# Kernel optimization log

Hardware: AMD Instinct MI355X
Metric: run time of the kernel (lower is better)

Reference implementation:

```python
import jax, jax.numpy as jnp
import numpy as np

G = 4  # number of groups


def _group_vals(h, shift, Ua, Ua1, Ua2, Ua3):
    # h: [B, H]; Ua: [g, H/g, r]; Ua1/2/3: [g, r, H/g]
    B, H = h.shape
    hg = h.reshape(B, G, H // G)
    if shift:
        # torch index = rotate-left by `shift`: new group j reads old group (j+shift)%g
        hg = jnp.roll(hg, -shift, axis=1)
    t = jnp.einsum('bgd,gdr->bgr', hg, Ua)  # shared low-rank projection
    proj = lambda M: jnp.einsum('bgr,grd->bgd', t, M).reshape(B, H)
    return proj(Ua1), proj(Ua2), proj(Ua3)


def setup_inputs() -> dict:
    key = jax.random.key(0)
    ks = jax.random.split(key, 24)
    B, I, H, wR = 8192, 1024, 1024, 256
    hg = H // G
    r01, r23 = 64, 32
    d = {}
    d['x'] = jax.random.normal(ks[0], (B, I), dtype=jnp.float32)
    d['h'] = jax.random.normal(ks[1], (B, H), dtype=jnp.float32)
    d['W'] = 0.1 * jax.random.normal(ks[2], (I, wR), dtype=jnp.float32)
    d['W1'] = 0.1 * jax.random.normal(ks[3], (wR, H), dtype=jnp.float32)
    d['W2'] = 0.1 * jax.random.normal(ks[4], (wR, H), dtype=jnp.float32)
    d['W3'] = 0.1 * jax.random.normal(ks[5], (wR, H), dtype=jnp.float32)
    d['U'] = 0.1 * jax.random.normal(ks[6], (G, hg, r01), dtype=jnp.float32)
    d['U1'] = 0.1 * jax.random.normal(ks[7], (G, r01, hg), dtype=jnp.float32)
    d['U2'] = 0.1 * jax.random.normal(ks[8], (G, r01, hg), dtype=jnp.float32)
    d['U3'] = 0.1 * jax.random.normal(ks[9], (G, r01, hg), dtype=jnp.float32)
    d['UU'] = 0.1 * jax.random.normal(ks[10], (G, hg, r01), dtype=jnp.float32)
    d['UU1'] = 0.1 * jax.random.normal(ks[11], (G, r01, hg), dtype=jnp.float32)
    d['UU2'] = 0.1 * jax.random.normal(ks[12], (G, r01, hg), dtype=jnp.float32)
    d['UU3'] = 0.1 * jax.random.normal(ks[13], (G, r01, hg), dtype=jnp.float32)
    d['UUU'] = 0.1 * jax.random.normal(ks[14], (G, hg, r23), dtype=jnp.float32)
    d['UUU1'] = 0.1 * jax.random.normal(ks[15], (G, r23, hg), dtype=jnp.float32)
    d['UUU2'] = 0.1 * jax.random.normal(ks[16], (G, r23, hg), dtype=jnp.float32)
    d['UUU3'] = 0.1 * jax.random.normal(ks[17], (G, r23, hg), dtype=jnp.float32)
    d['UUUU'] = 0.1 * jax.random.normal(ks[18], (G, hg, r23), dtype=jnp.float32)
    d['UUUU1'] = 0.1 * jax.random.normal(ks[19], (G, r23, hg), dtype=jnp.float32)
    d['UUUU2'] = 0.1 * jax.random.normal(ks[20], (G, r23, hg), dtype=jnp.float32)
    d['UUUU3'] = 0.1 * jax.random.normal(ks[21], (G, r23, hg), dtype=jnp.float32)
    d['bias_r'] = jnp.ones((1, H), dtype=jnp.float32)
    d['bias_gate'] = jnp.ones((1, H), dtype=jnp.float32)
    d['bias_update'] = jnp.ones((1, H), dtype=jnp.float32)
    return d


def reference(x, h, W, W1, W2, W3, U, U1, U2, U3, UU, UU1, UU2, UU3,
              UUU, UUU1, UUU2, UUU3, UUUU, UUUU1, UUUU2, UUUU3,
              bias_r, bias_gate, bias_update):
    u1, u2, u3 = _group_vals(h, 0, U, U1, U2, U3)
    uu1, uu2, uu3 = _group_vals(h, 1, UU, UU1, UU2, UU3)
    uuu1, uuu2, uuu3 = _group_vals(h, 2, UUU, UUU1, UUU2, UUU3)
    uuuu1, uuuu2, uuuu3 = _group_vals(h, 3, UUUU, UUUU1, UUUU2, UUUU3)
    xw = x @ W  # [B, wRank]
    w1, w2, w3 = xw @ W1, xw @ W2, xw @ W3
    r = jax.nn.sigmoid(w1 + u1 + uu1 + uuu1 + uuuu1 + bias_r)
    z = jax.nn.sigmoid(w2 + u2 + uu2 + uuu2 + uuuu2 + bias_gate)
    c_tilda = jnp.tanh(w3 + r * (u3 + uu3 + uuu3 + uuuu3) + bias_update)
    return z * h + (1.0 - z) * c_tilda
```

## Files before the change

kernel.cpp:

```cpp
#include <hip/hip_runtime.h>

typedef short bf16x8 __attribute__((ext_vector_type(8)));
typedef float f32x4 __attribute__((ext_vector_type(4)));

__device__ __forceinline__ unsigned short f2bf(float f) {
  union { float f; unsigned u; } c; c.f = f;
  unsigned u = c.u;
  u += 0x7FFFu + ((u >> 16) & 1u);
  return (unsigned short)(u >> 16);
}
__device__ __forceinline__ float bf2f(unsigned short h) {
  union { unsigned u; float f; } c; c.u = ((unsigned)h) << 16;
  return c.f;
}
__device__ __forceinline__ void split2(float v, unsigned short& hi, unsigned short& lo) {
  union { float f; unsigned u; } c; c.f = v;
  unsigned uh = c.u & 0xFFFF0000u;
  hi = (unsigned short)(uh >> 16);
  union { unsigned u; float f; } d; d.u = uh;
  lo = f2bf(v - d.f);
}
__device__ __forceinline__ void gload16(const void* g, void* l) {
  __builtin_amdgcn_global_load_lds((const __attribute__((address_space(1))) void*)g,
                                   (__attribute__((address_space(3))) void*)l, 16, 0, 0);
}
__device__ __forceinline__ float sigm(float x) { return 1.0f / (1.0f + __expf(-x)); }
__device__ __forceinline__ float tanha(float x) { return 1.0f - 2.0f / (1.0f + __expf(2.0f * x)); }

__global__ __launch_bounds__(256) void s123(
    const float* __restrict__ W,
    const float* __restrict__ U, const float* __restrict__ UU,
    const float* __restrict__ UUU, const float* __restrict__ UUUU,
    const float* __restrict__ W1, const float* __restrict__ W2, const float* __restrict__ W3,
    const float* __restrict__ A1, const float* __restrict__ A2, const float* __restrict__ A3,
    const float* __restrict__ B1, const float* __restrict__ B2, const float* __restrict__ B3,
    const float* __restrict__ C1, const float* __restrict__ C2, const float* __restrict__ C3,
    const float* __restrict__ D1, const float* __restrict__ D2, const float* __restrict__ D3,
    unsigned short* __restrict__ Wt, unsigned short* __restrict__ Bg,
    unsigned short* __restrict__ Bt) {
  int gidx = blockIdx.x * 256 + threadIdx.x;
  if (gidx < 262144) {
    int idx = gidx;
    int n = idx >> 10, k = idx & 1023;
    Wt[idx] = f2bf(W[k * 256 + n]);
  } else if (gidx < 458752) {
    int idx = gidx - 262144;
    int g = idx / 49152;
    int rem = idx - g * 49152;
    int n = rem >> 8, k = rem & 255;
    int jj = 0, rr = n;
#pragma unroll
    for (int s = 0; s < 3; ++s) {
      int w = (((g - jj) & 3) < 2) ? 64 : 32;
      if (rr >= w) { rr -= w; ++jj; }
    }
    int v = (g - jj) & 3;
    int rv = (v < 2) ? 64 : 32;
    const float* M = (v == 0) ? U : (v == 1) ? UU : (v == 2) ? UUU : UUUU;
    Bg[idx] = f2bf(M[(jj * 256 + k) * rv + rr]);
  } else {
    int idx = gidx - 458752;
    int j = idx / (1024 * 704);
    int rem = idx - j * (1024 * 704);
    int n = rem / 704, k = rem - n * 704;
    int p = n >> 8, c = n & 255;
    float val = 0.0f;
    if (k < 512) {
      int kk = k & 255;
      if (p == 0)      val = W1[kk * 1024 + j * 256 + c];
      else if (p == 1) val = W2[kk * 1024 + j * 256 + c];
      else if (p == 2) val = W3[kk * 1024 + j * 256 + c];
    } else if (p != 2) {
      int k2 = k - 512;
      int v, off, rv;
      if (k2 < 64)       { v = 0; off = 0;   rv = 64; }
      else if (k2 < 128) { v = 1; off = 64;  rv = 64; }
      else if (k2 < 160) { v = 2; off = 128; rv = 32; }
      else               { v = 3; off = 160; rv = 32; }
      int r = k2 - off;
      int pp = (p == 3) ? 2 : p;
      const float* M;
      if (v == 0)      M = (pp == 0) ? A1 : (pp == 1) ? A2 : A3;
      else if (v == 1) M = (pp == 0) ? B1 : (pp == 1) ? B2 : B3;
      else if (v == 2) M = (pp == 0) ? C1 : (pp == 1) ? C2 : C3;
      else             M = (pp == 0) ? D1 : (pp == 1) ? D2 : D3;
      val = M[(j * rv + r) * 256 + c];
    }
    Bt[idx] = f2bf(val);
  }
}

__global__ __launch_bounds__(256) void g1_xw(const float* __restrict__ x,
                                             const unsigned short* __restrict__ Wt,
                                             unsigned short* __restrict__ Abuf) {
  __shared__ char lds[49152];
  const int tid = threadIdx.x, lane = tid & 63, wid = tid >> 6;
  const int mb = blockIdx.x, nb = blockIdx.y;
  const int wn = wid;
  f32x4 acc[2][2] = {};
  float4 xr[2];
  const int r0 = tid >> 4, f4c = tid & 15;
  const float* xbase = x + (size_t)(mb * 32) * 1024 + f4c * 4;

  auto loadX = [&](int kt) {
#pragma unroll
    for (int q = 0; q < 2; ++q)
      xr[q] = *(const float4*)(xbase + (size_t)(q * 16 + r0) * 1024 + kt * 64);
  };
  auto writeA = [&](int buf) {
#pragma unroll
    for (int q = 0; q < 2; ++q) {
      int row = q * 16 + r0;
      float4 v = xr[q];
      unsigned short h0, h1, h2, h3, l0, l1, l2, l3;
      split2(v.x, h0, l0); split2(v.y, h1, l1);
      split2(v.z, h2, l2); split2(v.w, h3, l3);
      int ba = row * 128 + ((f4c * 8) ^ ((row & 7) << 4));
      *(uint2*)(lds + buf * 4096 + ba) =
          make_uint2(((unsigned)h1 << 16) | h0, ((unsigned)h3 << 16) | h2);
      *(uint2*)(lds + 8192 + buf * 4096 + ba) =
          make_uint2(((unsigned)l1 << 16) | l0, ((unsigned)l3 << 16) | l2);
    }
  };
  auto stageB = [&](int kt, int buf) {
#pragma unroll
    for (int it = 0; it < 4; ++it) {
      int nloc = it * 32 + wid * 8 + (lane >> 3);
      const char* src = (const char*)Wt + (size_t)(nb * 128 + nloc) * 2048 + kt * 128
                        + (((lane & 7) * 16) ^ ((nloc & 7) << 4));
      gload16(src, lds + 16384 + buf * 16384 + it * 4096 + wid * 1024);
    }
  };

  loadX(0); stageB(0, 0); writeA(0);
  __syncthreads();
#pragma unroll 2
  for (int kt = 0; kt < 16; ++kt) {
    int buf = kt & 1;
    if (kt < 15) { loadX(kt + 1); stageB(kt + 1, buf ^ 1); }
    const char* hA = lds + buf * 4096;
    const char* lA = lds + 8192 + buf * 4096;
    const char* bB = lds + 16384 + buf * 16384;
#pragma unroll
    for (int ks = 0; ks < 2; ++ks) {
      bf16x8 ah[2], al[2], b[2];
#pragma unroll
      for (int mf = 0; mf < 2; ++mf) {
        int mloc = mf * 16 + (lane & 15);
        int ka = (ks * 64 + (lane >> 4) * 16) ^ ((mloc & 7) << 4);
        ah[mf] = *(const bf16x8*)(hA + mloc * 128 + ka);
        al[mf] = *(const bf16x8*)(lA + mloc * 128 + ka);
      }
#pragma unroll
      for (int nf = 0; nf < 2; ++nf) {
        int nloc = wn * 32 + nf * 16 + (lane & 15);
        int kb = (ks * 64 + (lane >> 4) * 16) ^ ((nloc & 7) << 4);
        b[nf] = *(const bf16x8*)(bB + nloc * 128 + kb);
      }
#pragma unroll
      for (int mf = 0; mf < 2; ++mf)
#pragma unroll
        for (int nf = 0; nf < 2; ++nf) {
          acc[mf][nf] = __builtin_amdgcn_mfma_f32_16x16x32_bf16(ah[mf], b[nf], acc[mf][nf], 0, 0, 0);
          acc[mf][nf] = __builtin_amdgcn_mfma_f32_16x16x32_bf16(al[mf], b[nf], acc[mf][nf], 0, 0, 0);
        }
    }
    if (kt < 15) writeA(buf ^ 1);
    __syncthreads();
  }
#pragma unroll
  for (int mf = 0; mf < 2; ++mf)
#pragma unroll
    for (int nf = 0; nf < 2; ++nf)
#pragma unroll
      for (int r = 0; r < 4; ++r) {
        int row = mb * 32 + mf * 16 + (lane >> 4) * 4 + r;
        int col = nb * 128 + wn * 32 + nf * 16 + (lane & 15);
        float val = acc[mf][nf][r];
        unsigned short hi, lo;
        split2(val, hi, lo);
        Abuf[(size_t)row * 1280 + col] = hi;
        Abuf[(size_t)row * 1280 + 256 + col] = lo;
      }
}

__global__ __launch_bounds__(256) void g2_t(const float* __restrict__ h,
                                            const unsigned short* __restrict__ Bg,
                                            unsigned short* __restrict__ Abuf) {
  __shared__ char lds[65536];
  const int tid = threadIdx.x, lane = tid & 63, wid = tid >> 6;
  const int mb = blockIdx.x, g = blockIdx.y;
  const int wm = wid >> 1, wn = wid & 1;
  f32x4 acc[2][6] = {};
  float4 hr[4];
  const int r0 = tid >> 4, f4c = tid & 15;
  const float* hbase = h + (size_t)(mb * 64) * 1024 + g * 256 + f4c * 4;

  auto loadH = [&](int kt) {
#pragma unroll
    for (int q = 0; q < 4; ++q)
      hr[q] = *(const float4*)(hbase + (size_t)(q * 16 + r0) * 1024 + kt * 64);
  };
  auto writeA = [&](int buf) {
#pragma unroll
    for (int q = 0; q < 4; ++q) {
      int row = q * 16 + r0;
      float4 v = hr[q];
      int ba = row * 128 + ((f4c * 8) ^ ((row & 7) << 4));
      *(uint2*)(lds + buf * 8192 + ba) =
          make_uint2(((unsigned)f2bf(v.y) << 16) | f2bf(v.x),
                     ((unsigned)f2bf(v.w) << 16) | f2bf(v.z));
    }
  };
  auto stageB = [&](int kt, int buf) {
#pragma unroll
    for (int it = 0; it < 6; ++it) {
      int nloc = it * 32 + wid * 8 + (lane >> 3);
      const char* src = (const char*)Bg + (size_t)(g * 192 + nloc) * 512 + kt * 128
                        + (((lane & 7) * 16) ^ ((nloc & 7) << 4));
      gload16(src, lds + 16384 + buf * 24576 + it * 4096 + wid * 1024);
    }
  };

  loadH(0); stageB(0, 0); writeA(0);
  __syncthreads();
#pragma unroll
  for (int kt = 0; kt < 4; ++kt) {
    int buf = kt & 1;
    if (kt < 3) { loadH(kt + 1); stageB(kt + 1, buf ^ 1); }
    const char* cA = lds + buf * 8192;
    const char* cB = lds + 16384 + buf * 24576;
#pragma unroll
    for (int ks = 0; ks < 2; ++ks) {
      bf16x8 a[2], b[6];
#pragma unroll
      for (int mf = 0; mf < 2; ++mf) {
        int mloc = wm * 32 + mf * 16 + (lane & 15);
        int ka = (ks * 64 + (lane >> 4) * 16) ^ ((mloc & 7) << 4);
        a[mf] = *(const bf16x8*)(cA + mloc * 128 + ka);
      }
#pragma unroll
      for (int nf = 0; nf < 6; ++nf) {
        int nloc = wn * 96 + nf * 16 + (lane & 15);
        int kb = (ks * 64 + (lane >> 4) * 16) ^ ((nloc & 7) << 4);
        b[nf] = *(const bf16x8*)(cB + nloc * 128 + kb);
      }
#pragma unroll
      for (int mf = 0; mf < 2; ++mf)
#pragma unroll
        for (int nf = 0; nf < 6; ++nf)
          acc[mf][nf] = __builtin_amdgcn_mfma_f32_16x16x32_bf16(a[mf], b[nf], acc[mf][nf], 0, 0, 0);
    }
    if (kt < 3) writeA(buf ^ 1);
    __syncthreads();
  }
#pragma unroll
  for (int mf = 0; mf < 2; ++mf)
#pragma unroll
    for (int nf = 0; nf < 6; ++nf) {
      int n = wn * 96 + nf * 16 + (lane & 15);
      int jj = 0, rr = n;
#pragma unroll
      for (int s = 0; s < 3; ++s) {
        int w = (((g - jj) & 3) < 2) ? 64 : 32;
        if (rr >= w) { rr -= w; ++jj; }
      }
      int v = (g - jj) & 3;
      int offv = (v < 2) ? (v << 6) : (64 + (v << 5));
      int col = 512 + jj * 192 + offv + rr;
#pragma unroll
      for (int r = 0; r < 4; ++r) {
        int row = mb * 64 + wm * 32 + mf * 16 + (lane >> 4) * 4 + r;
        Abuf[(size_t)row * 1280 + col] = f2bf(acc[mf][nf][r]);
      }
    }
}

__global__ __launch_bounds__(256) void g3_main(const unsigned short* __restrict__ Abuf,
                                               const unsigned short* __restrict__ Bt,
                                               const float* __restrict__ h,
                                               const float* __restrict__ bias_r,
                                               const float* __restrict__ bias_g,
                                               const float* __restrict__ bias_u,
                                               float* __restrict__ out) {
  __shared__ char lds[65536];
  const int tid = threadIdx.x, lane = tid & 63, wid = tid >> 6;
  const int mb = blockIdx.x, nb = blockIdx.y, j = blockIdx.z;
  const int wm = wid >> 1, wn = wid & 1;
  f32x4 acc[4][4] = {};

  const char* AbufB = (const char*)Abuf + (size_t)mb * 128 * 2560;
  const char* BtB = (const char*)Bt + (size_t)j * 1441792;
  int thrA[4], thrB[4], dstOff[4];
#pragma unroll
  for (int it = 0; it < 4; ++it) {
    int mloc = wid * 32 + it * 8 + (lane >> 3);
    int swz = ((lane & 7) * 16) ^ ((mloc & 7) << 4);
    thrA[it] = mloc * 2560 + swz;
    int cb2 = (mloc >> 6) & 1, p = (mloc >> 4) & 3, c16 = mloc & 15;
    thrB[it] = (p * 256 + nb * 32 + cb2 * 16 + c16) * 1408 + swz;
    dstOff[it] = wid * 4096 + it * 1024;
  }
  const char* pA[4][2];
  const char* pB[4][2];
#pragma unroll
  for (int mf = 0; mf < 4; ++mf) {
    int mloc = wm * 64 + mf * 16 + (lane & 15);
#pragma unroll
    for (int ks = 0; ks < 2; ++ks) {
      int ka = (ks * 64 + (lane >> 4) * 16) ^ ((mloc & 7) << 4);
      pA[mf][ks] = lds + mloc * 128 + ka;
    }
  }
#pragma unroll
  for (int p = 0; p < 4; ++p) {
    int nloc = wn * 64 + p * 16 + (lane & 15);
#pragma unroll
    for (int ks = 0; ks < 2; ++ks) {
      int kb = (ks * 64 + (lane >> 4) * 16) ^ ((nloc & 7) << 4);
      pB[p][ks] = lds + 32768 + nloc * 128 + kb;
    }
  }

  auto stage = [&](int kt, int buf) {
    int colb2 = (kt < 8) ? kt * 128 : (1024 + j * 384 + (kt - 8) * 128);
#pragma unroll
    for (int it = 0; it < 4; ++it)
      gload16(AbufB + colb2 + thrA[it], lds + buf * 16384 + dstOff[it]);
#pragma unroll
    for (int it = 0; it < 4; ++it)
      gload16(BtB + kt * 128 + thrB[it], lds + 32768 + buf * 16384 + dstOff[it]);
  };

  stage(0, 0);
  __syncthreads();
#pragma unroll
  for (int kt = 0; kt < 11; ++kt) {
    int buf = kt & 1;
    if (kt < 10) stage(kt + 1, buf ^ 1);
    __builtin_amdgcn_s_setprio(1);
#pragma unroll
    for (int ks = 0; ks < 2; ++ks) {
      bf16x8 a[4];
#pragma unroll
      for (int mf = 0; mf < 4; ++mf)
        a[mf] = *(const bf16x8*)(pA[mf][ks] + buf * 16384);
#pragma unroll
      for (int p = 0; p < 4; ++p) {
        if (p == 2 && kt >= 8) continue;
        if (p == 3 && kt < 8) continue;
        bf16x8 b = *(const bf16x8*)(pB[p][ks] + buf * 16384);
#pragma unroll
        for (int mf = 0; mf < 4; ++mf)
          acc[mf][p] = __builtin_amdgcn_mfma_f32_16x16x32_bf16(a[mf], b, acc[mf][p], 0, 0, 0);
      }
    }
    __builtin_amdgcn_s_setprio(0);
    __syncthreads();
  }
  int cg = j * 256 + nb * 32 + wn * 16 + (lane & 15);
  float br = bias_r[cg], bg = bias_g[cg], bu = bias_u[cg];
#pragma unroll
  for (int mf = 0; mf < 4; ++mf)
#pragma unroll
    for (int r = 0; r < 4; ++r) {
      int row = mb * 128 + wm * 64 + mf * 16 + (lane >> 4) * 4 + r;
      float p0 = acc[mf][0][r], p1 = acc[mf][1][r];
      float p2 = acc[mf][2][r], p3 = acc[mf][3][r];
      float rr = sigm(p0 + br);
      float zz = sigm(p1 + bg);
      float ct = tanha(p2 + rr * p3 + bu);
      float hv = h[(size_t)row * 1024 + cg];
      out[(size_t)row * 1024 + cg] = zz * hv + (1.0f - zz) * ct;
    }
}

extern "C" void kernel_launch(void* const* d_in, const int* in_sizes, int n_in,
                              void* d_out, int out_size, void* d_ws, size_t ws_size,
                              hipStream_t stream) {
  const float* x   = (const float*)d_in[0];
  const float* h   = (const float*)d_in[1];
  const float* W   = (const float*)d_in[2];
  const float* W1  = (const float*)d_in[3];
  const float* W2  = (const float*)d_in[4];
  const float* W3  = (const float*)d_in[5];
  const float* U   = (const float*)d_in[6];
  const float* U1  = (const float*)d_in[7];
  const float* U2  = (const float*)d_in[8];
  const float* U3  = (const float*)d_in[9];
  const float* UU   = (const float*)d_in[10];
  const float* UU1  = (const float*)d_in[11];
  const float* UU2  = (const float*)d_in[12];
  const float* UU3  = (const float*)d_in[13];
  const float* UUU   = (const float*)d_in[14];
  const float* UUU1  = (const float*)d_in[15];
  const float* UUU2  = (const float*)d_in[16];
  const float* UUU3  = (const float*)d_in[17];
  const float* UUUU   = (const float*)d_in[18];
  const float* UUUU1  = (const float*)d_in[19];
  const float* UUUU2  = (const float*)d_in[20];
  const float* UUUU3  = (const float*)d_in[21];
  const float* bias_r = (const float*)d_in[22];
  const float* bias_g = (const float*)d_in[23];
  const float* bias_u = (const float*)d_in[24];

  char* ws = (char*)d_ws;
  unsigned short* Abuf = (unsigned short*)(ws);
  unsigned short* Wt   = (unsigned short*)(ws + 20971520);
  unsigned short* Bg   = (unsigned short*)(ws + 21495808);
  unsigned short* Bt   = (unsigned short*)(ws + 21889024);
  float* out = (float*)d_out;

  s123<<<13056, 256, 0, stream>>>(W, U, UU, UUU, UUUU,
                                  W1, W2, W3, U1, U2, U3, UU1, UU2, UU3,
                                  UUU1, UUU2, UUU3, UUUU1, UUUU2, UUUU3,
                                  Wt, Bg, Bt);
  g1_xw<<<dim3(256, 2), 256, 0, stream>>>(x, Wt, Abuf);
  g2_t<<<dim3(128, 4), 256, 0, stream>>>(h, Bg, Abuf);
  g3_main<<<dim3(64, 8, 4), 256, 0, stream>>>(Abuf, Bt, h, bias_r, bias_g, bias_u, out);
}
```

Baseline: 99.98 us.

## Pack weight tiles contiguously, drop zero-padded B slots, and pipeline with explicit waitcnts

```diff
diff --git a/kernel.cpp b/kernel.cpp
--- a/kernel.cpp
+++ b/kernel.cpp
@@ -37,7 +37,7 @@
     const float* __restrict__ C1, const float* __restrict__ C2, const float* __restrict__ C3,
     const float* __restrict__ D1, const float* __restrict__ D2, const float* __restrict__ D3,
     unsigned short* __restrict__ Wt, unsigned short* __restrict__ Bg,
-    unsigned short* __restrict__ Bt) {
+    unsigned short* __restrict__ Btp) {
   int gidx = blockIdx.x * 256 + threadIdx.x;
   if (gidx < 262144) {
     int idx = gidx;
@@ -60,33 +60,37 @@
     Bg[idx] = f2bf(M[(jj * 256 + k) * rv + rr]);
   } else {
     int idx = gidx - 458752;
-    int j = idx / (1024 * 704);
-    int rem = idx - j * (1024 * 704);
-    int n = rem / 704, k = rem - n * 704;
-    int p = n >> 8, c = n & 255;
-    float val = 0.0f;
-    if (k < 512) {
-      int kk = k & 255;
-      if (p == 0)      val = W1[kk * 1024 + j * 256 + c];
-      else if (p == 1) val = W2[kk * 1024 + j * 256 + c];
-      else if (p == 2) val = W3[kk * 1024 + j * 256 + c];
-    } else if (p != 2) {
-      int k2 = k - 512;
-      int v, off, rv;
-      if (k2 < 64)       { v = 0; off = 0;   rv = 64; }
-      else if (k2 < 128) { v = 1; off = 64;  rv = 64; }
-      else if (k2 < 160) { v = 2; off = 128; rv = 32; }
-      else               { v = 3; off = 160; rv = 32; }
-      int r = k2 - off;
-      int pp = (p == 3) ? 2 : p;
+    int j  = idx / 540672;
+    int r1 = idx - j * 540672;
+    int kt = r1 / 49152;
+    int r2 = r1 - kt * 49152;
+    int c2 = r2 / 3072;
+    int r3 = r2 - c2 * 3072;
+    int q  = r3 >> 10;
+    int r4 = r3 & 1023;
+    int c16 = r4 >> 6;
+    int k2  = r4 & 63;
+    int c = c2 * 16 + c16;
+    float val;
+    if (kt < 8) {
+      int kk = (kt * 64 + k2) & 255;
+      const float* Wp = (q == 0) ? W1 : (q == 1) ? W2 : W3;
+      val = Wp[kk * 1024 + j * 256 + c];
+    } else {
+      int kT = (kt - 8) * 64 + k2;
+      int v, r, rv;
+      if (kT < 64)       { v = 0; r = kT;       rv = 64; }
+      else if (kT < 128) { v = 1; r = kT - 64;  rv = 64; }
+      else if (kT < 160) { v = 2; r = kT - 128; rv = 32; }
+      else               { v = 3; r = kT - 160; rv = 32; }
       const float* M;
-      if (v == 0)      M = (pp == 0) ? A1 : (pp == 1) ? A2 : A3;
-      else if (v == 1) M = (pp == 0) ? B1 : (pp == 1) ? B2 : B3;
-      else if (v == 2) M = (pp == 0) ? C1 : (pp == 1) ? C2 : C3;
-      else             M = (pp == 0) ? D1 : (pp == 1) ? D2 : D3;
+      if (v == 0)      M = (q == 0) ? A1 : (q == 1) ? A2 : A3;
+      else if (v == 1) M = (q == 0) ? B1 : (q == 1) ? B2 : B3;
+      else if (v == 2) M = (q == 0) ? C1 : (q == 1) ? C2 : C3;
+      else             M = (q == 0) ? D1 : (q == 1) ? D2 : D3;
       val = M[(j * rv + r) * 256 + c];
     }
-    Bt[idx] = f2bf(val);
+    Btp[idx] = f2bf(val);
   }
 }
 
@@ -128,7 +132,7 @@
       int nloc = it * 32 + wid * 8 + (lane >> 3);
       const char* src = (const char*)Wt + (size_t)(nb * 128 + nloc) * 2048 + kt * 128
                         + (((lane & 7) * 16) ^ ((nloc & 7) << 4));
-      gload16(src, lds + 16384 + buf * 16384 + it * 4096 + wid * 1024);
+      gload16(src, lds + 16384 + buf * 16384 + (it * 32 + wid * 8) * 128);
     }
   };
 
@@ -137,7 +141,14 @@
 #pragma unroll 2
   for (int kt = 0; kt < 16; ++kt) {
     int buf = kt & 1;
-    if (kt < 15) { loadX(kt + 1); stageB(kt + 1, buf ^ 1); }
+    if (kt < 15) {
+      loadX(kt + 1); stageB(kt + 1, buf ^ 1);
+      asm volatile("s_waitcnt vmcnt(6)" ::: "memory");
+    } else {
+      asm volatile("s_waitcnt vmcnt(0)" ::: "memory");
+    }
+    __builtin_amdgcn_s_barrier();
+    __builtin_amdgcn_sched_barrier(0);
     const char* hA = lds + buf * 4096;
     const char* lA = lds + 8192 + buf * 4096;
     const char* bB = lds + 16384 + buf * 16384;
@@ -166,7 +177,9 @@
         }
     }
     if (kt < 15) writeA(buf ^ 1);
-    __syncthreads();
+    __builtin_amdgcn_sched_barrier(0);
+    asm volatile("s_waitcnt lgkmcnt(0)" ::: "memory");
+    __builtin_amdgcn_s_barrier();
   }
 #pragma unroll
   for (int mf = 0; mf < 2; ++mf)
@@ -218,7 +231,7 @@
       int nloc = it * 32 + wid * 8 + (lane >> 3);
       const char* src = (const char*)Bg + (size_t)(g * 192 + nloc) * 512 + kt * 128
                         + (((lane & 7) * 16) ^ ((nloc & 7) << 4));
-      gload16(src, lds + 16384 + buf * 24576 + it * 4096 + wid * 1024);
+      gload16(src, lds + 16384 + buf * 24576 + (it * 32 + wid * 8) * 128);
     }
   };
 
@@ -277,67 +290,73 @@
 }
 
 __global__ __launch_bounds__(256) void g3_main(const unsigned short* __restrict__ Abuf,
-                                               const unsigned short* __restrict__ Bt,
+                                               const unsigned short* __restrict__ Btp,
                                                const float* __restrict__ h,
                                                const float* __restrict__ bias_r,
                                                const float* __restrict__ bias_g,
                                                const float* __restrict__ bias_u,
                                                float* __restrict__ out) {
-  __shared__ char lds[65536];
+  __shared__ char lds[57344];
   const int tid = threadIdx.x, lane = tid & 63, wid = tid >> 6;
   const int mb = blockIdx.x, nb = blockIdx.y, j = blockIdx.z;
   const int wm = wid >> 1, wn = wid & 1;
   f32x4 acc[4][4] = {};
 
   const char* AbufB = (const char*)Abuf + (size_t)mb * 128 * 2560;
-  const char* BtB = (const char*)Bt + (size_t)j * 1441792;
-  int thrA[4], thrB[4], dstOff[4];
+  const char* BtpJ  = (const char*)Btp + (size_t)j * 1081344;
+  int thrA[4], dstA[4], thrB[3], dstB[3];
 #pragma unroll
   for (int it = 0; it < 4; ++it) {
     int mloc = wid * 32 + it * 8 + (lane >> 3);
-    int swz = ((lane & 7) * 16) ^ ((mloc & 7) << 4);
-    thrA[it] = mloc * 2560 + swz;
-    int cb2 = (mloc >> 6) & 1, p = (mloc >> 4) & 3, c16 = mloc & 15;
-    thrB[it] = (p * 256 + nb * 32 + cb2 * 16 + c16) * 1408 + swz;
-    dstOff[it] = wid * 4096 + it * 1024;
+    thrA[it] = mloc * 2560 + (((lane & 7) * 16) ^ ((mloc & 7) << 4));
+    dstA[it] = wid * 4096 + it * 1024;
+  }
+#pragma unroll
+  for (int it = 0; it < 3; ++it) {
+    int row = it * 32 + wid * 8 + (lane >> 3);
+    thrB[it] = row * 128 + (((lane & 7) * 16) ^ ((row & 7) << 4));
+    dstB[it] = (it * 32 + wid * 8) * 128;
   }
   const char* pA[4][2];
-  const char* pB[4][2];
+  const char* pB[3][2];
 #pragma unroll
   for (int mf = 0; mf < 4; ++mf) {
     int mloc = wm * 64 + mf * 16 + (lane & 15);
 #pragma unroll
-    for (int ks = 0; ks < 2; ++ks) {
-      int ka = (ks * 64 + (lane >> 4) * 16) ^ ((mloc & 7) << 4);
-      pA[mf][ks] = lds + mloc * 128 + ka;
-    }
-  }
-#pragma unroll
-  for (int p = 0; p < 4; ++p) {
-    int nloc = wn * 64 + p * 16 + (lane & 15);
-#pragma unroll
-    for (int ks = 0; ks < 2; ++ks) {
-      int kb = (ks * 64 + (lane >> 4) * 16) ^ ((nloc & 7) << 4);
-      pB[p][ks] = lds + 32768 + nloc * 128 + kb;
-    }
+    for (int ks = 0; ks < 2; ++ks)
+      pA[mf][ks] = lds + mloc * 128 + ((ks * 64 + (lane >> 4) * 16) ^ ((mloc & 7) << 4));
+  }
+#pragma unroll
+  for (int q = 0; q < 3; ++q) {
+    int nloc = wn * 48 + q * 16 + (lane & 15);
+#pragma unroll
+    for (int ks = 0; ks < 2; ++ks)
+      pB[q][ks] = lds + 32768 + nloc * 128 + ((ks * 64 + (lane >> 4) * 16) ^ ((nloc & 7) << 4));
   }
 
   auto stage = [&](int kt, int buf) {
     int colb2 = (kt < 8) ? kt * 128 : (1024 + j * 384 + (kt - 8) * 128);
 #pragma unroll
     for (int it = 0; it < 4; ++it)
-      gload16(AbufB + colb2 + thrA[it], lds + buf * 16384 + dstOff[it]);
-#pragma unroll
-    for (int it = 0; it < 4; ++it)
-      gload16(BtB + kt * 128 + thrB[it], lds + 32768 + buf * 16384 + dstOff[it]);
+      gload16(AbufB + colb2 + thrA[it], lds + buf * 16384 + dstA[it]);
+    const char* bsrc = BtpJ + (size_t)(kt * 16 + nb * 2) * 6144;
+#pragma unroll
+    for (int it = 0; it < 3; ++it)
+      gload16(bsrc + thrB[it], lds + 32768 + buf * 12288 + dstB[it]);
   };
 
   stage(0, 0);
-  __syncthreads();
 #pragma unroll
   for (int kt = 0; kt < 11; ++kt) {
     int buf = kt & 1;
-    if (kt < 10) stage(kt + 1, buf ^ 1);
+    if (kt < 10) {
+      stage(kt + 1, buf ^ 1);
+      asm volatile("s_waitcnt vmcnt(7)" ::: "memory");
+    } else {
+      asm volatile("s_waitcnt vmcnt(0)" ::: "memory");
+    }
+    __builtin_amdgcn_s_barrier();
+    __builtin_amdgcn_sched_barrier(0);
     __builtin_amdgcn_s_setprio(1);
 #pragma unroll
     for (int ks = 0; ks < 2; ++ks) {
@@ -346,17 +365,18 @@
       for (int mf = 0; mf < 4; ++mf)
         a[mf] = *(const bf16x8*)(pA[mf][ks] + buf * 16384);
 #pragma unroll
-      for (int p = 0; p < 4; ++p) {
-        if (p == 2 && kt >= 8) continue;
-        if (p == 3 && kt < 8) continue;
-        bf16x8 b = *(const bf16x8*)(pB[p][ks] + buf * 16384);
+      for (int q = 0; q < 3; ++q) {
+        int p = (kt < 8) ? q : ((q == 2) ? 3 : q);
+        bf16x8 b = *(const bf16x8*)(pB[q][ks] + buf * 12288);
 #pragma unroll
         for (int mf = 0; mf < 4; ++mf)
           acc[mf][p] = __builtin_amdgcn_mfma_f32_16x16x32_bf16(a[mf], b, acc[mf][p], 0, 0, 0);
       }
     }
     __builtin_amdgcn_s_setprio(0);
-    __syncthreads();
+    __builtin_amdgcn_sched_barrier(0);
+    asm volatile("s_waitcnt lgkmcnt(0)" ::: "memory");
+    __builtin_amdgcn_s_barrier();
   }
   int cg = j * 256 + nb * 32 + wn * 16 + (lane & 15);
   float br = bias_r[cg], bg = bias_g[cg], bu = bias_u[cg];
@@ -408,14 +428,14 @@
   unsigned short* Abuf = (unsigned short*)(ws);
   unsigned short* Wt   = (unsigned short*)(ws + 20971520);
   unsigned short* Bg   = (unsigned short*)(ws + 21495808);
-  unsigned short* Bt   = (unsigned short*)(ws + 21889024);
+  unsigned short* Btp  = (unsigned short*)(ws + 21889024);
   float* out = (float*)d_out;
 
-  s123<<<13056, 256, 0, stream>>>(W, U, UU, UUU, UUUU,
+  s123<<<10240, 256, 0, stream>>>(W, U, UU, UUU, UUUU,
                                   W1, W2, W3, U1, U2, U3, UU1, UU2, UU3,
                                   UUU1, UUU2, UUU3, UUUU1, UUUU2, UUUU3,
-                                  Wt, Bg, Bt);
+                                  Wt, Bg, Btp);
   g1_xw<<<dim3(256, 2), 256, 0, stream>>>(x, Wt, Abuf);
   g2_t<<<dim3(128, 4), 256, 0, stream>>>(h, Bg, Abuf);
-  g3_main<<<dim3(64, 8, 4), 256, 0, stream>>>(Abuf, Bt, h, bias_r, bias_g, bias_u, out);
-}
+  g3_main<<<dim3(64, 8, 4), 256, 0, stream>>>(Abuf, Btp, h, bias_r, bias_g, bias_u, out);
+}
```

Result: faster. 97.08 us (-2.9%).
